# Performance work log

Hardware: AMD Instinct MI355X
Metric: run time of the kernel (lower is better)

Reference implementation:

```python
import jax, jax.numpy as jnp
import numpy as np

N, E, G, H, F_IN = 100_000, 3_200_000, 256, 16, 7
RRELU_SLOPE = (1.0 / 8.0 + 1.0 / 3.0) / 2.0  # eval-mode RReLU uses mean slope


def rrelu(x):
    return jnp.where(x >= 0, x, RRELU_SLOPE * x)


def gcn_conv(x, edge_index, edge_weight, W, b, n_nodes):
    """PyG GCNConv: add self-loops, symmetric norm, gather-matmul-scatter."""
    row, col = edge_index[0], edge_index[1]
    loop = jnp.arange(n_nodes)
    row = jnp.concatenate([row, loop])
    col = jnp.concatenate([col, loop])
    w = jnp.concatenate([edge_weight, jnp.ones((n_nodes,), x.dtype)])
    deg = jax.ops.segment_sum(w, col, num_segments=n_nodes)
    dis = jnp.where(deg > 0, jax.lax.rsqrt(jnp.maximum(deg, 1e-12)), 0.0)
    norm = dis[row] * w * dis[col]            # [E+N]
    h = x @ W                                  # [N, out]
    msg = h[row] * norm[:, None]               # gather + scale
    return jax.ops.segment_sum(msg, col, num_segments=n_nodes) + b


def max_pool_neighbor_x(x, edge_index, n_nodes):
    row, col = edge_index[0], edge_index[1]
    loop = jnp.arange(n_nodes)
    row = jnp.concatenate([row, loop])
    col = jnp.concatenate([col, loop])
    return jax.ops.segment_max(x[row], col, num_segments=n_nodes)


def setup_inputs() -> dict:
    key = jax.random.key(0)
    ks = jax.random.split(key, 12)
    x = jax.random.normal(ks[0], (N, F_IN), jnp.float32)
    edge_index = jax.random.randint(ks[1], (2, E), 0, N)
    edge_weights = jax.random.uniform(ks[2], (E,), jnp.float32)
    batch = (jnp.arange(N) * G) // N  # sorted, every graph non-empty
    s = 0.2
    W1 = jax.random.normal(ks[3], (F_IN, H), jnp.float32) * s
    b1 = jnp.zeros((H,), jnp.float32)
    W2 = jax.random.normal(ks[4], (H, H), jnp.float32) * s
    b2 = jnp.zeros((H,), jnp.float32)
    Wl1 = jax.random.normal(ks[5], (H, H), jnp.float32) * s
    bl1 = jax.random.normal(ks[6], (H,), jnp.float32) * s
    Wl3 = jax.random.normal(ks[7], (H, H), jnp.float32) * s
    bl3 = jax.random.normal(ks[8], (H,), jnp.float32) * s
    Wl4 = jax.random.normal(ks[9], (H, 1), jnp.float32) * s
    bl4 = jax.random.normal(ks[10], (1,), jnp.float32) * s
    return {"x": x, "edge_index": edge_index, "batch": batch,
            "edge_weights": edge_weights, "W1": W1, "b1": b1, "W2": W2,
            "b2": b2, "Wl1": Wl1, "bl1": bl1, "Wl3": Wl3, "bl3": bl3,
            "Wl4": Wl4, "bl4": bl4}


def reference(x, edge_index, batch, edge_weights, W1, b1, W2, b2,
              Wl1, bl1, Wl3, bl3, Wl4, bl4):
    h = gcn_conv(x, edge_index, edge_weights, W1, b1, N)
    h = max_pool_neighbor_x(h, edge_index, N)
    res = h
    h = gcn_conv(h, edge_index, jnp.ones((E,), h.dtype), W2, b2, N)
    h = jax.nn.relu(res + h)
    g = jax.ops.segment_max(h, batch, num_segments=G)  # global_max_pool
    res = g
    g = rrelu(res + (g @ Wl1 + bl1))
    res = g
    g = rrelu(res + (g @ Wl3 + bl3))
    # dropout p=0.5 in eval mode -> identity
    g = rrelu(g @ Wl4 + bl4)
    return g
```

## Files before the change

kernel.cpp:

```cpp
#include <hip/hip_runtime.h>
#include <hip/hip_fp16.h>
#include <math.h>

#define NN 100000
#define NE 3200000
#define NG 256
#define HD 16
#define FIN 7

#define RB 8
#define RSZ 256
#define NBUK 391
#define NBUKP 400
#define FB 1024
#define CHUNK 3125
#define SCB 8
#define ASTRIDE 17
#define CSTRIDE 9
#define LMASK 0x1FFFF

#define S16 65536.0f
#define INV_S16 1.52587890625e-5f
#define IBIAS 33554432u
#define S_DEGW 16777216.0f
#define INV_S_DEGW 5.9604644775390625e-8f

static constexpr float SLOPE = 0.22916666666666666f;

__device__ __forceinline__ float rrelu_f(float a) {
    return a >= 0.f ? a : SLOPE * a;
}

__device__ __forceinline__ unsigned encf(float v) {
    unsigned u = __float_as_uint(v);
    return u ^ (((unsigned)((int)u >> 31)) | 0x80000000u);
}
__device__ __forceinline__ float decf(unsigned u) {
    unsigned m = ((int)u < 0) ? 0x80000000u : 0xFFFFFFFFu;
    return __uint_as_float(u ^ m);
}
#define ENC_NEGINF 0x00800000u

__device__ __forceinline__ float h2f(unsigned short us) {
    __half h = *(__half*)&us;
    return __half2float(h);
}

__global__ __launch_bounds__(256) void k_hist(
        const int* __restrict__ col, int* __restrict__ hist) {
    __shared__ int bins[NBUK];
    for (int i = threadIdx.x; i < NBUK; i += 256) bins[i] = 0;
    __syncthreads();
    int base = blockIdx.x * CHUNK;
    for (int i = threadIdx.x; i < CHUNK; i += 256)
        atomicAdd(&bins[col[base + i] >> RB], 1);
    __syncthreads();
    for (int i = threadIdx.x; i < NBUK; i += 256)
        hist[blockIdx.x * NBUKP + i] = bins[i];
}

__global__ __launch_bounds__(512) void k_scan_a(
        const int* __restrict__ hist, int* __restrict__ pre_t,
        int* __restrict__ tot) {
    __shared__ int s[SCB * (FB + 1)];
    int t = threadIdx.x;
    int c0 = blockIdx.x * SCB;
    for (int i = t; i < SCB * FB; i += 512) {
        int j = i >> 3, c = i & 7;
        int cc = c0 + c;
        s[c * (FB + 1) + j] = (cc < NBUK) ? hist[j * NBUKP + cc] : 0;
    }
    __syncthreads();
    int w = t >> 6, l = t & 63;
    int* sb = &s[w * (FB + 1)];
    int base = l * 16;
    int loc[16];
    int run = 0;
#pragma unroll
    for (int k = 0; k < 16; ++k) { loc[k] = run; run += sb[base + k]; }
    int inc = run;
#pragma unroll
    for (int d = 1; d < 64; d <<= 1) {
        int v = __shfl_up(inc, d, 64);
        if (l >= d) inc += v;
    }
    int excl = inc - run;
    int cc = c0 + w;
    if (cc < NBUK) {
#pragma unroll
        for (int k = 0; k < 16; ++k) sb[base + k] = excl + loc[k];
        if (l == 63) tot[cc] = inc;
    }
    __syncthreads();
    for (int i = t; i < SCB * FB; i += 512) {
        int j = i >> 3, c = i & 7;
        int cc2 = c0 + c;
        if (cc2 < NBUK) pre_t[j * NBUKP + cc2] = s[c * (FB + 1) + j];
    }
}

__global__ __launch_bounds__(512) void k_scan_b(
        const int* __restrict__ tot, int* __restrict__ bstart) {
    __shared__ int s[512];
    int t = threadIdx.x;
    int v = (t < NBUK) ? tot[t] : 0;
    s[t] = v;
    __syncthreads();
    for (int d = 1; d < 512; d <<= 1) {
        int add = (t >= d) ? s[t - d] : 0;
        __syncthreads();
        s[t] += add;
        __syncthreads();
    }
    if (t < NBUK) bstart[t + 1] = s[t];
    if (t == 0) bstart[0] = 0;
}

__global__ __launch_bounds__(256) void k_fill(
        const int* __restrict__ row, const int* __restrict__ col,
        const float* __restrict__ ew,
        const int* __restrict__ pre_t, const int* __restrict__ bstart,
        unsigned* __restrict__ sp, unsigned short* __restrict__ swh) {
    __shared__ int lcnt[NBUK];
    __shared__ int gofs[NBUK];
    __shared__ int part[256];
    __shared__ unsigned ssp[CHUNK];
    __shared__ unsigned short ssw[CHUNK];
    __shared__ unsigned short sbuk[CHUNK];
    int t = threadIdx.x;
    for (int i = t; i < NBUK; i += 256) {
        lcnt[i] = 0;
        gofs[i] = bstart[i] + pre_t[blockIdx.x * NBUKP + i];
    }
    __syncthreads();
    int base = blockIdx.x * CHUNK;
    for (int i = t; i < CHUNK; i += 256)
        atomicAdd(&lcnt[col[base + i] >> RB], 1);
    __syncthreads();
    int k0 = t * 2;
    int c0 = (k0 + 0 < NBUK) ? lcnt[k0 + 0] : 0;
    int c1 = (k0 + 1 < NBUK) ? lcnt[k0 + 1] : 0;
    int gsum = c0 + c1;
    part[t] = gsum;
    __syncthreads();
    for (int d = 1; d < 256; d <<= 1) {
        int add = (t >= d) ? part[t - d] : 0;
        __syncthreads();
        part[t] += add;
        __syncthreads();
    }
    {
        int run = part[t] - gsum;
        int e0 = run, e1 = run + c0;
        if (k0 + 0 < NBUK) { gofs[k0 + 0] -= e0; lcnt[k0 + 0] = e0; }
        if (k0 + 1 < NBUK) { gofs[k0 + 1] -= e1; lcnt[k0 + 1] = e1; }
    }
    __syncthreads();
    for (int i = t; i < CHUNK; i += 256) {
        int c = col[base + i];
        int b = c >> RB;
        int s = atomicAdd(&lcnt[b], 1);
        ssp[s] = ((unsigned)(c & (RSZ - 1)) << 17) | (unsigned)row[base + i];
        __half hv = __float2half_rn(ew[base + i]);
        ssw[s] = *(unsigned short*)&hv;
        sbuk[s] = (unsigned short)b;
    }
    __syncthreads();
    for (int s = t; s < CHUNK; s += 256) {
        int g = s + gofs[sbuk[s]];
        sp[g] = ssp[s];
        swh[g] = ssw[s];
    }
}

__global__ __launch_bounds__(1024) void k_deg(
        const unsigned* __restrict__ sp, const unsigned short* __restrict__ swh,
        const int* __restrict__ bstart,
        const float* __restrict__ x, const float* __restrict__ W1,
        float* __restrict__ h1, float* __restrict__ dis1,
        float* __restrict__ dis2, int* __restrict__ cnts,
        unsigned* __restrict__ h1h) {
    __shared__ unsigned long long sdeg[RSZ];
    __shared__ float sdis[RSZ];
    __shared__ float sW1[FIN * HD];
    int t = threadIdx.x;
    if (t < FIN * HD) sW1[t] = W1[t];
    if (t < RSZ) sdeg[t] = 0ULL;
    __syncthreads();
    int s0 = bstart[blockIdx.x], s1 = bstart[blockIdx.x + 1];
    int j = s0 + t;
    for (; j + 3072 < s1; j += 4096) {
        unsigned e0 = sp[j], e1 = sp[j + 1024], e2 = sp[j + 2048], e3 = sp[j + 3072];
        float w0 = h2f(swh[j]), w1 = h2f(swh[j + 1024]);
        float w2 = h2f(swh[j + 2048]), w3 = h2f(swh[j + 3072]);
        atomicAdd(&sdeg[e0 >> 17], (1ULL << 32) |
                  (unsigned long long)(unsigned)__float2int_rn(w0 * S_DEGW));
        atomicAdd(&sdeg[e1 >> 17], (1ULL << 32) |
                  (unsigned long long)(unsigned)__float2int_rn(w1 * S_DEGW));
        atomicAdd(&sdeg[e2 >> 17], (1ULL << 32) |
                  (unsigned long long)(unsigned)__float2int_rn(w2 * S_DEGW));
        atomicAdd(&sdeg[e3 >> 17], (1ULL << 32) |
                  (unsigned long long)(unsigned)__float2int_rn(w3 * S_DEGW));
    }
    for (; j < s1; j += 1024) {
        unsigned e = sp[j];
        float w = h2f(swh[j]);
        atomicAdd(&sdeg[e >> 17], (1ULL << 32) |
                  (unsigned long long)(unsigned)__float2int_rn(w * S_DEGW));
    }
    __syncthreads();
    int node0 = blockIdx.x * RSZ;
    if (t < RSZ && node0 + t < NN) {
        unsigned long long v = sdeg[t];
        unsigned cnt = (unsigned)(v >> 32);
        float wsum = (float)(unsigned)(v & 0xFFFFFFFFULL) * INV_S_DEGW;
        float d1 = rsqrtf(wsum + 1.f);
        dis1[node0 + t] = d1;
        sdis[t] = d1;
        dis2[node0 + t] = rsqrtf((float)cnt + 1.f);
        cnts[node0 + t] = (int)cnt;
    }
    __syncthreads();
    for (int i = t; i < RSZ * 8; i += 1024) {
        int ln = i >> 3, p = i & 7;
        int node = node0 + ln;
        if (node < NN) {
            float a0 = 0.f, a1 = 0.f;
#pragma unroll
            for (int k = 0; k < FIN; ++k) {
                float xv = x[node * FIN + k];
                a0 += xv * sW1[k * HD + 2 * p];
                a1 += xv * sW1[k * HD + 2 * p + 1];
            }
            h1[node * HD + 2 * p] = a0;
            h1[node * HD + 2 * p + 1] = a1;
            float d = sdis[ln];
            __half2 hh = __floats2half2_rn(a0 * d, a1 * d);
            h1h[node * 8 + p] = *(unsigned*)&hh;
        }
    }
}

__device__ __forceinline__ void conv_acc2(unsigned long long* acc, unsigned ex,
                                          uint2 g, float w, int p2) {
    float2 fa = __half22float2(*(__half2*)&g.x);
    float2 fb = __half22float2(*(__half2*)&g.y);
    unsigned qa0 = (unsigned)__float2int_rn(fa.x * w) + IBIAS;
    unsigned qa1 = (unsigned)__float2int_rn(fa.y * w) + IBIAS;
    unsigned qb0 = (unsigned)__float2int_rn(fb.x * w) + IBIAS;
    unsigned qb1 = (unsigned)__float2int_rn(fb.y * w) + IBIAS;
    int lc = ex >> 17;
    atomicAdd(&acc[lc * CSTRIDE + 2 * p2],
              ((unsigned long long)qa0 << 32) | (unsigned long long)qa1);
    atomicAdd(&acc[lc * CSTRIDE + 2 * p2 + 1],
              ((unsigned long long)qb0 << 32) | (unsigned long long)qb1);
}

__global__ __launch_bounds__(1024) void k_conv1(
        const unsigned* __restrict__ sp, const unsigned short* __restrict__ swh,
        const int* __restrict__ bstart,
        const unsigned* __restrict__ h1h, const float* __restrict__ h1,
        const float* __restrict__ dis1, const int* __restrict__ cnts,
        const float* __restrict__ b1, unsigned* __restrict__ h1outh) {
    __shared__ unsigned long long acc[RSZ * CSTRIDE];
    int t = threadIdx.x;
    for (int i = t; i < RSZ * CSTRIDE; i += 1024) acc[i] = 0ULL;
    __syncthreads();
    int p2 = t & 3, slot = t >> 2;
    const uint2* h1h2 = (const uint2*)h1h;
    int s0 = bstart[blockIdx.x], s1 = bstart[blockIdx.x + 1];
    int j = s0 + slot;
    for (; j + 768 < s1; j += 1024) {
        unsigned e0 = sp[j], e1 = sp[j + 256], e2 = sp[j + 512], e3 = sp[j + 768];
        float w0 = h2f(swh[j]) * S16, w1 = h2f(swh[j + 256]) * S16;
        float w2 = h2f(swh[j + 512]) * S16, w3 = h2f(swh[j + 768]) * S16;
        uint2 g0 = h1h2[(e0 & LMASK) * 4 + p2];
        uint2 g1 = h1h2[(e1 & LMASK) * 4 + p2];
        uint2 g2 = h1h2[(e2 & LMASK) * 4 + p2];
        uint2 g3 = h1h2[(e3 & LMASK) * 4 + p2];
        conv_acc2(acc, e0, g0, w0, p2);
        conv_acc2(acc, e1, g1, w1, p2);
        conv_acc2(acc, e2, g2, w2, p2);
        conv_acc2(acc, e3, g3, w3, p2);
    }
    for (; j < s1; j += 256) {
        unsigned e = sp[j];
        float w = h2f(swh[j]) * S16;
        uint2 g = h1h2[(e & LMASK) * 4 + p2];
        conv_acc2(acc, e, g, w, p2);
    }
    __syncthreads();
    int node0 = blockIdx.x * RSZ;
    for (int i = t; i < RSZ * 8; i += 1024) {
        int ln = i >> 3, pp = i & 7;
        int node = node0 + ln;
        if (node < NN) {
            unsigned long long v = acc[ln * CSTRIDE + pp];
            unsigned kb = (unsigned)cnts[node] * IBIAS;
            float a0 = (float)(int)((unsigned)(v >> 32) - kb) * INV_S16;
            float a1 = (float)(int)((unsigned)(v & 0xFFFFFFFFULL) - kb) * INV_S16;
            float d = dis1[node];
            float r0 = a0 * d + h1[node * HD + 2 * pp] * d * d + b1[2 * pp];
            float r1 = a1 * d + h1[node * HD + 2 * pp + 1] * d * d + b1[2 * pp + 1];
            __half2 hh = __floats2half2_rn(r0, r1);
            h1outh[node * 8 + pp] = *(unsigned*)&hh;
        }
    }
}

__global__ __launch_bounds__(1024) void k_pool_h2(
        const unsigned* __restrict__ sp, const int* __restrict__ bstart,
        const unsigned* __restrict__ h1outh, const float* __restrict__ W2,
        const float* __restrict__ dis2,
        float2* __restrict__ pool2, float2* __restrict__ h2s,
        unsigned* __restrict__ h2sh) {
    __shared__ unsigned acc[RSZ * ASTRIDE];
    __shared__ float sW2[256];
    int t = threadIdx.x;
    if (t < 256) sW2[t] = W2[t];
    for (int i = t; i < RSZ * ASTRIDE; i += 1024) acc[i] = ENC_NEGINF;
    __syncthreads();
    int p2 = t & 3, slot = t >> 2;
    const uint2* hv2 = (const uint2*)h1outh;
    int s0 = bstart[blockIdx.x], s1 = bstart[blockIdx.x + 1];
    int j = s0 + slot;
    for (; j + 768 < s1; j += 1024) {
        unsigned e0 = sp[j], e1 = sp[j + 256], e2 = sp[j + 512], e3 = sp[j + 768];
        uint2 g0 = hv2[(e0 & LMASK) * 4 + p2];
        uint2 g1 = hv2[(e1 & LMASK) * 4 + p2];
        uint2 g2 = hv2[(e2 & LMASK) * 4 + p2];
        uint2 g3 = hv2[(e3 & LMASK) * 4 + p2];
        float2 f;
        unsigned* a;
        a = &acc[(e0 >> 17) * ASTRIDE + 4 * p2];
        f = __half22float2(*(__half2*)&g0.x);
        atomicMax(a + 0, encf(f.x)); atomicMax(a + 1, encf(f.y));
        f = __half22float2(*(__half2*)&g0.y);
        atomicMax(a + 2, encf(f.x)); atomicMax(a + 3, encf(f.y));
        a = &acc[(e1 >> 17) * ASTRIDE + 4 * p2];
        f = __half22float2(*(__half2*)&g1.x);
        atomicMax(a + 0, encf(f.x)); atomicMax(a + 1, encf(f.y));
        f = __half22float2(*(__half2*)&g1.y);
        atomicMax(a + 2, encf(f.x)); atomicMax(a + 3, encf(f.y));
        a = &acc[(e2 >> 17) * ASTRIDE + 4 * p2];
        f = __half22float2(*(__half2*)&g2.x);
        atomicMax(a + 0, encf(f.x)); atomicMax(a + 1, encf(f.y));
        f = __half22float2(*(__half2*)&g2.y);
        atomicMax(a + 2, encf(f.x)); atomicMax(a + 3, encf(f.y));
        a = &acc[(e3 >> 17) * ASTRIDE + 4 * p2];
        f = __half22float2(*(__half2*)&g3.x);
        atomicMax(a + 0, encf(f.x)); atomicMax(a + 1, encf(f.y));
        f = __half22float2(*(__half2*)&g3.y);
        atomicMax(a + 2, encf(f.x)); atomicMax(a + 3, encf(f.y));
    }
    for (; j < s1; j += 256) {
        unsigned e = sp[j];
        uint2 g = hv2[(e & LMASK) * 4 + p2];
        unsigned* a = &acc[(e >> 17) * ASTRIDE + 4 * p2];
        float2 f = __half22float2(*(__half2*)&g.x);
        atomicMax(a + 0, encf(f.x)); atomicMax(a + 1, encf(f.y));
        f = __half22float2(*(__half2*)&g.y);
        atomicMax(a + 2, encf(f.x)); atomicMax(a + 3, encf(f.y));
    }
    __syncthreads();
    int node0 = blockIdx.x * RSZ;
    for (int i = t; i < RSZ * 8; i += 1024) {
        int ln = i >> 3, pp = i & 7;
        int node = node0 + ln;
        if (node < NN) {
            unsigned sh = h1outh[node * 8 + pp];
            float2 sf = __half22float2(*(__half2*)&sh);
            float m0 = fmaxf(decf(acc[ln * ASTRIDE + 2 * pp]),     sf.x);
            float m1 = fmaxf(decf(acc[ln * ASTRIDE + 2 * pp + 1]), sf.y);
            pool2[node * 8 + pp] = make_float2(m0, m1);
            acc[ln * ASTRIDE + 2 * pp]     = __float_as_uint(m0);
            acc[ln * ASTRIDE + 2 * pp + 1] = __float_as_uint(m1);
        }
    }
    __syncthreads();
    for (int i = t; i < RSZ * 8; i += 1024) {
        int ln = i >> 3, pp = i & 7;
        int node = node0 + ln;
        if (node < NN) {
            float a0 = 0.f, a1 = 0.f;
#pragma unroll
            for (int k = 0; k < HD; ++k) {
                float pv = __uint_as_float(acc[ln * ASTRIDE + k]);
                a0 += pv * sW2[k * HD + 2 * pp];
                a1 += pv * sW2[k * HD + 2 * pp + 1];
            }
            float d = dis2[node];
            a0 *= d; a1 *= d;
            h2s[node * 8 + pp] = make_float2(a0, a1);
            __half2 hh = __floats2half2_rn(a0, a1);
            h2sh[node * 8 + pp] = *(unsigned*)&hh;
        }
    }
}

__global__ __launch_bounds__(1024) void k_conv2(
        const unsigned* __restrict__ sp, const int* __restrict__ bstart,
        const unsigned* __restrict__ h2sh, const float2* __restrict__ h2s,
        const float* __restrict__ dis2, const int* __restrict__ cnts,
        const float2* __restrict__ pool2, const float* __restrict__ b2,
        float2* __restrict__ hfin2) {
    __shared__ unsigned long long acc[RSZ * CSTRIDE];
    int t = threadIdx.x;
    for (int i = t; i < RSZ * CSTRIDE; i += 1024) acc[i] = 0ULL;
    __syncthreads();
    int p2 = t & 3, slot = t >> 2;
    const uint2* hv2 = (const uint2*)h2sh;
    int s0 = bstart[blockIdx.x], s1 = bstart[blockIdx.x + 1];
    int j = s0 + slot;
    for (; j + 768 < s1; j += 1024) {
        unsigned e0 = sp[j], e1 = sp[j + 256], e2 = sp[j + 512], e3 = sp[j + 768];
        uint2 g0 = hv2[(e0 & LMASK) * 4 + p2];
        uint2 g1 = hv2[(e1 & LMASK) * 4 + p2];
        uint2 g2 = hv2[(e2 & LMASK) * 4 + p2];
        uint2 g3 = hv2[(e3 & LMASK) * 4 + p2];
        conv_acc2(acc, e0, g0, S16, p2);
        conv_acc2(acc, e1, g1, S16, p2);
        conv_acc2(acc, e2, g2, S16, p2);
        conv_acc2(acc, e3, g3, S16, p2);
    }
    for (; j < s1; j += 256) {
        unsigned e = sp[j];
        uint2 g = hv2[(e & LMASK) * 4 + p2];
        conv_acc2(acc, e, g, S16, p2);
    }
    __syncthreads();
    int node0 = blockIdx.x * RSZ;
    for (int i = t; i < RSZ * 8; i += 1024) {
        int ln = i >> 3, pp = i & 7;
        int node = node0 + ln;
        if (node < NN) {
            unsigned long long v = acc[ln * CSTRIDE + pp];
            unsigned kb = (unsigned)cnts[node] * IBIAS;
            float a0 = (float)(int)((unsigned)(v >> 32) - kb) * INV_S16;
            float a1 = (float)(int)((unsigned)(v & 0xFFFFFFFFULL) - kb) * INV_S16;
            float d = dis2[node];
            float2 self = h2s[node * 8 + pp];
            float2 pl = pool2[node * 8 + pp];
            float r0 = pl.x + (a0 + self.x) * d + b2[2 * pp];
            float r1 = pl.y + (a1 + self.y) * d + b2[2 * pp + 1];
            hfin2[node * 8 + pp] = make_float2(fmaxf(r0, 0.f), fmaxf(r1, 0.f));
        }
    }
}

__global__ __launch_bounds__(256) void k_graph_max(
        const float* __restrict__ hfin, float* __restrict__ gbuf) {
    int g = blockIdx.x;
    int start = (g * NN + NG - 1) / NG;
    int end   = ((g + 1) * NN + NG - 1) / NG;
    int f = threadIdx.x & 15, sub = threadIdx.x >> 4;
    float m = -3.402823466e38f;
    for (int i = start + sub; i < end; i += 16)
        m = fmaxf(m, hfin[i * HD + f]);
    __shared__ float lds[256];
    lds[threadIdx.x] = m;
    __syncthreads();
    if (threadIdx.x < 16) {
        float mm = lds[threadIdx.x];
#pragma unroll
        for (int s = 1; s < 16; ++s) mm = fmaxf(mm, lds[s * 16 + threadIdx.x]);
        gbuf[g * HD + threadIdx.x] = mm;
    }
}

__global__ __launch_bounds__(256) void k_mlp(
        const float* __restrict__ gbuf,
        const float* __restrict__ Wl1, const float* __restrict__ bl1,
        const float* __restrict__ Wl3, const float* __restrict__ bl3,
        const float* __restrict__ Wl4, const float* __restrict__ bl4,
        float* __restrict__ out) {
    __shared__ float sW1[256], sW3[256], sW4[16], sb1[16], sb3[16];
    __shared__ float sb4;
    int tid = threadIdx.x;
    sW1[tid] = Wl1[tid];
    sW3[tid] = Wl3[tid];
    if (tid < 16) { sW4[tid] = Wl4[tid]; sb1[tid] = bl1[tid]; sb3[tid] = bl3[tid]; }
    if (tid == 0) sb4 = bl4[0];
    __syncthreads();

    float v[16], t1[16], t2[16];
#pragma unroll
    for (int f = 0; f < 16; ++f) v[f] = gbuf[tid * 16 + f];
#pragma unroll
    for (int f = 0; f < 16; ++f) {
        float a = sb1[f] + v[f];
#pragma unroll
        for (int k = 0; k < 16; ++k) a += v[k] * sW1[k * 16 + f];
        t1[f] = rrelu_f(a);
    }
#pragma unroll
    for (int f = 0; f < 16; ++f) {
        float a = sb3[f] + t1[f];
#pragma unroll
        for (int k = 0; k < 16; ++k) a += t1[k] * sW3[k * 16 + f];
        t2[f] = rrelu_f(a);
    }
    float o = sb4;
#pragma unroll
    for (int k = 0; k < 16; ++k) o += t2[k] * sW4[k];
    out[tid] = rrelu_f(o);
}

extern "C" void kernel_launch(void* const* d_in, const int* in_sizes, int n_in,
                              void* d_out, int out_size, void* d_ws, size_t ws_size,
                              hipStream_t stream) {
    const float* x   = (const float*)d_in[0];
    const int*   ei  = (const int*)  d_in[1];
    const float* ew  = (const float*)d_in[3];
    const float* W1  = (const float*)d_in[4];
    const float* b1  = (const float*)d_in[5];
    const float* W2  = (const float*)d_in[6];
    const float* b2  = (const float*)d_in[7];
    const float* Wl1 = (const float*)d_in[8];
    const float* bl1 = (const float*)d_in[9];
    const float* Wl3 = (const float*)d_in[10];
    const float* bl3 = (const float*)d_in[11];
    const float* Wl4 = (const float*)d_in[12];
    const float* bl4 = (const float*)d_in[13];
    const int* row = ei;
    const int* col = ei + NE;

    float* ws = (float*)d_ws;
    float* h1    = ws;
    float* pool  = h1   + NN * HD;
    float* h2s   = pool + NN * HD;
    float* dis1  = h2s  + NN * HD;
    float* dis2  = dis1 + NN;
    int*   cnts  = (int*)(dis2 + NN);
    float* gbuf  = (float*)(cnts + NN);
    unsigned* h1h    = (unsigned*)(gbuf + NG * HD);
    unsigned* h1outh = h1h    + NN * 8;
    unsigned* h2sh   = h1outh + NN * 8;
    unsigned* sp     = h2sh   + NN * 8;
    unsigned short* swh = (unsigned short*)(sp + NE);
    int* tot    = (int*)(swh + NE + (NE & 1));
    int* bstart = tot + NBUK;
    int* hist   = (int*)pool;
    int* pre_t  = (int*)h2s;
    float* hfin = h1;

    const int B = 256;

    k_hist     <<<FB, B, 0, stream>>>(col, hist);
    k_scan_a   <<<(NBUK + SCB - 1) / SCB, 512, 0, stream>>>(hist, pre_t, tot);
    k_scan_b   <<<1, 512, 0, stream>>>(tot, bstart);
    k_fill     <<<FB, B, 0, stream>>>(row, col, ew, pre_t, bstart, sp, swh);
    k_deg      <<<NBUK, 1024, 0, stream>>>(sp, swh, bstart, x, W1, h1,
                                           dis1, dis2, cnts, h1h);
    k_conv1    <<<NBUK, 1024, 0, stream>>>(sp, swh, bstart, h1h, h1, dis1,
                                           cnts, b1, h1outh);
    k_pool_h2  <<<NBUK, 1024, 0, stream>>>(sp, bstart, h1outh, W2, dis2,
                                           (float2*)pool, (float2*)h2s, h2sh);
    k_conv2    <<<NBUK, 1024, 0, stream>>>(sp, bstart, h2sh, (const float2*)h2s, dis2,
                                           cnts, (const float2*)pool, b2, (float2*)hfin);
    k_graph_max<<<NG, B, 0, stream>>>(hfin, gbuf);
    k_mlp      <<<1, B, 0, stream>>>(gbuf, Wl1, bl1, Wl3, bl3, Wl4, bl4, (float*)d_out);
}
```

Baseline: 259.5 us.

## Build per-node CSR and replace LDS atomic aggregation with per-node register reductions

After: 316.8 us. 22.1% more time.

```diff
diff --git a/kernel.cpp b/kernel.cpp
--- a/kernel.cpp
+++ b/kernel.cpp
@@ -16,12 +16,8 @@
 #define CHUNK 3125
 #define SCB 8
 #define ASTRIDE 17
-#define CSTRIDE 9
 #define LMASK 0x1FFFF
 
-#define S16 65536.0f
-#define INV_S16 1.52587890625e-5f
-#define IBIAS 33554432u
 #define S_DEGW 16777216.0f
 #define INV_S_DEGW 5.9604644775390625e-8f
 
@@ -30,16 +26,6 @@
 __device__ __forceinline__ float rrelu_f(float a) {
     return a >= 0.f ? a : SLOPE * a;
 }
-
-__device__ __forceinline__ unsigned encf(float v) {
-    unsigned u = __float_as_uint(v);
-    return u ^ (((unsigned)((int)u >> 31)) | 0x80000000u);
-}
-__device__ __forceinline__ float decf(unsigned u) {
-    unsigned m = ((int)u < 0) ? 0x80000000u : 0xFFFFFFFFu;
-    return __uint_as_float(u ^ m);
-}
-#define ENC_NEGINF 0x00800000u
 
 __device__ __forceinline__ float h2f(unsigned short us) {
     __half h = *(__half*)&us;
@@ -173,279 +159,233 @@
     }
 }
 
-__global__ __launch_bounds__(1024) void k_deg(
+__global__ __launch_bounds__(1024) void k_sort2(
         const unsigned* __restrict__ sp, const unsigned short* __restrict__ swh,
         const int* __restrict__ bstart,
         const float* __restrict__ x, const float* __restrict__ W1,
-        float* __restrict__ h1, float* __restrict__ dis1,
-        float* __restrict__ dis2, int* __restrict__ cnts,
-        unsigned* __restrict__ h1h) {
-    __shared__ unsigned long long sdeg[RSZ];
+        unsigned* __restrict__ sp2, unsigned short* __restrict__ sw2,
+        int* __restrict__ rowptr, float* __restrict__ dis1,
+        float* __restrict__ dis2, unsigned* __restrict__ h1h) {
+    __shared__ int scnt[RSZ];
+    __shared__ int stmp[RSZ];
+    __shared__ int soff[RSZ + 1];
+    __shared__ int walker[RSZ];
+    __shared__ unsigned wsum[RSZ];
     __shared__ float sdis[RSZ];
     __shared__ float sW1[FIN * HD];
     int t = threadIdx.x;
     if (t < FIN * HD) sW1[t] = W1[t];
-    if (t < RSZ) sdeg[t] = 0ULL;
+    if (t < RSZ) { scnt[t] = 0; walker[t] = 0; wsum[t] = 0u; }
     __syncthreads();
     int s0 = bstart[blockIdx.x], s1 = bstart[blockIdx.x + 1];
-    int j = s0 + t;
-    for (; j + 3072 < s1; j += 4096) {
-        unsigned e0 = sp[j], e1 = sp[j + 1024], e2 = sp[j + 2048], e3 = sp[j + 3072];
-        float w0 = h2f(swh[j]), w1 = h2f(swh[j + 1024]);
-        float w2 = h2f(swh[j + 2048]), w3 = h2f(swh[j + 3072]);
-        atomicAdd(&sdeg[e0 >> 17], (1ULL << 32) |
-                  (unsigned long long)(unsigned)__float2int_rn(w0 * S_DEGW));
-        atomicAdd(&sdeg[e1 >> 17], (1ULL << 32) |
-                  (unsigned long long)(unsigned)__float2int_rn(w1 * S_DEGW));
-        atomicAdd(&sdeg[e2 >> 17], (1ULL << 32) |
-                  (unsigned long long)(unsigned)__float2int_rn(w2 * S_DEGW));
-        atomicAdd(&sdeg[e3 >> 17], (1ULL << 32) |
-                  (unsigned long long)(unsigned)__float2int_rn(w3 * S_DEGW));
-    }
-    for (; j < s1; j += 1024) {
+    for (int j = s0 + t; j < s1; j += 1024)
+        atomicAdd(&scnt[sp[j] >> 17], 1);
+    __syncthreads();
+    int c = (t < RSZ) ? scnt[t] : 0;
+    if (t < RSZ) stmp[t] = c;
+    __syncthreads();
+    for (int d = 1; d < RSZ; d <<= 1) {
+        int v = (t < RSZ && t >= d) ? stmp[t - d] : 0;
+        __syncthreads();
+        if (t < RSZ) stmp[t] += v;
+        __syncthreads();
+    }
+    if (t < RSZ) soff[t] = stmp[t] - c;
+    if (t == 0) soff[RSZ] = s1 - s0;
+    __syncthreads();
+    int node0 = blockIdx.x * RSZ;
+    for (int i = t; i <= RSZ; i += 1024) {
+        int node = node0 + i;
+        if (node <= NN) rowptr[node] = s0 + soff[i];
+    }
+    for (int j = s0 + t; j < s1; j += 1024) {
         unsigned e = sp[j];
-        float w = h2f(swh[j]);
-        atomicAdd(&sdeg[e >> 17], (1ULL << 32) |
-                  (unsigned long long)(unsigned)__float2int_rn(w * S_DEGW));
-    }
-    __syncthreads();
-    int node0 = blockIdx.x * RSZ;
-    if (t < RSZ && node0 + t < NN) {
-        unsigned long long v = sdeg[t];
-        unsigned cnt = (unsigned)(v >> 32);
-        float wsum = (float)(unsigned)(v & 0xFFFFFFFFULL) * INV_S_DEGW;
-        float d1 = rsqrtf(wsum + 1.f);
-        dis1[node0 + t] = d1;
-        sdis[t] = d1;
-        dis2[node0 + t] = rsqrtf((float)cnt + 1.f);
-        cnts[node0 + t] = (int)cnt;
-    }
-    __syncthreads();
-    for (int i = t; i < RSZ * 8; i += 1024) {
-        int ln = i >> 3, p = i & 7;
+        unsigned short w = swh[j];
+        int lc = e >> 17;
+        int pos = s0 + soff[lc] + atomicAdd(&walker[lc], 1);
+        sp2[pos] = e & LMASK;
+        sw2[pos] = w;
+        atomicAdd(&wsum[lc], (unsigned)__float2int_rn(h2f(w) * S_DEGW));
+    }
+    __syncthreads();
+    if (t < RSZ) {
+        int node = node0 + t;
+        if (node < NN) {
+            float wsumf = (float)wsum[t] * INV_S_DEGW;
+            float d1 = rsqrtf(wsumf + 1.f);
+            dis1[node] = d1;
+            sdis[t] = d1;
+            dis2[node] = rsqrtf((float)scnt[t] + 1.f);
+        }
+    }
+    __syncthreads();
+    uint2* h1h2 = (uint2*)h1h;
+    for (int i = t; i < RSZ * 4; i += 1024) {
+        int ln = i >> 2, p2 = i & 3;
         int node = node0 + ln;
         if (node < NN) {
-            float a0 = 0.f, a1 = 0.f;
+            float a0 = 0.f, a1 = 0.f, a2 = 0.f, a3 = 0.f;
 #pragma unroll
             for (int k = 0; k < FIN; ++k) {
                 float xv = x[node * FIN + k];
-                a0 += xv * sW1[k * HD + 2 * p];
-                a1 += xv * sW1[k * HD + 2 * p + 1];
+                a0 += xv * sW1[k * HD + 4 * p2 + 0];
+                a1 += xv * sW1[k * HD + 4 * p2 + 1];
+                a2 += xv * sW1[k * HD + 4 * p2 + 2];
+                a3 += xv * sW1[k * HD + 4 * p2 + 3];
             }
-            h1[node * HD + 2 * p] = a0;
-            h1[node * HD + 2 * p + 1] = a1;
             float d = sdis[ln];
-            __half2 hh = __floats2half2_rn(a0 * d, a1 * d);
-            h1h[node * 8 + p] = *(unsigned*)&hh;
+            __half2 ha = __floats2half2_rn(a0 * d, a1 * d);
+            __half2 hb = __floats2half2_rn(a2 * d, a3 * d);
+            h1h2[node * 4 + p2] = make_uint2(*(unsigned*)&ha, *(unsigned*)&hb);
         }
     }
 }
 
-__device__ __forceinline__ void conv_acc2(unsigned long long* acc, unsigned ex,
-                                          uint2 g, float w, int p2) {
-    float2 fa = __half22float2(*(__half2*)&g.x);
-    float2 fb = __half22float2(*(__half2*)&g.y);
-    unsigned qa0 = (unsigned)__float2int_rn(fa.x * w) + IBIAS;
-    unsigned qa1 = (unsigned)__float2int_rn(fa.y * w) + IBIAS;
-    unsigned qb0 = (unsigned)__float2int_rn(fb.x * w) + IBIAS;
-    unsigned qb1 = (unsigned)__float2int_rn(fb.y * w) + IBIAS;
-    int lc = ex >> 17;
-    atomicAdd(&acc[lc * CSTRIDE + 2 * p2],
-              ((unsigned long long)qa0 << 32) | (unsigned long long)qa1);
-    atomicAdd(&acc[lc * CSTRIDE + 2 * p2 + 1],
-              ((unsigned long long)qb0 << 32) | (unsigned long long)qb1);
-}
+#define ACCW(g, w) { \
+    float2 fa_ = __half22float2(*(__half2*)&(g).x); \
+    float2 fb_ = __half22float2(*(__half2*)&(g).y); \
+    a0 += fa_.x * (w); a1 += fa_.y * (w); a2 += fb_.x * (w); a3 += fb_.y * (w); }
+
+#define ACCS(g) { \
+    float2 fa_ = __half22float2(*(__half2*)&(g).x); \
+    float2 fb_ = __half22float2(*(__half2*)&(g).y); \
+    a0 += fa_.x; a1 += fa_.y; a2 += fb_.x; a3 += fb_.y; }
+
+#define ACCM(g) { \
+    float2 fa_ = __half22float2(*(__half2*)&(g).x); \
+    float2 fb_ = __half22float2(*(__half2*)&(g).y); \
+    a0 = fmaxf(a0, fa_.x); a1 = fmaxf(a1, fa_.y); \
+    a2 = fmaxf(a2, fb_.x); a3 = fmaxf(a3, fb_.y); }
 
 __global__ __launch_bounds__(1024) void k_conv1(
-        const unsigned* __restrict__ sp, const unsigned short* __restrict__ swh,
-        const int* __restrict__ bstart,
-        const unsigned* __restrict__ h1h, const float* __restrict__ h1,
-        const float* __restrict__ dis1, const int* __restrict__ cnts,
+        const unsigned* __restrict__ sp2, const unsigned short* __restrict__ sw2,
+        const int* __restrict__ rowptr,
+        const unsigned* __restrict__ h1h, const float* __restrict__ dis1,
         const float* __restrict__ b1, unsigned* __restrict__ h1outh) {
-    __shared__ unsigned long long acc[RSZ * CSTRIDE];
-    int t = threadIdx.x;
-    for (int i = t; i < RSZ * CSTRIDE; i += 1024) acc[i] = 0ULL;
-    __syncthreads();
-    int p2 = t & 3, slot = t >> 2;
-    const uint2* h1h2 = (const uint2*)h1h;
-    int s0 = bstart[blockIdx.x], s1 = bstart[blockIdx.x + 1];
-    int j = s0 + slot;
-    for (; j + 768 < s1; j += 1024) {
-        unsigned e0 = sp[j], e1 = sp[j + 256], e2 = sp[j + 512], e3 = sp[j + 768];
-        float w0 = h2f(swh[j]) * S16, w1 = h2f(swh[j + 256]) * S16;
-        float w2 = h2f(swh[j + 512]) * S16, w3 = h2f(swh[j + 768]) * S16;
-        uint2 g0 = h1h2[(e0 & LMASK) * 4 + p2];
-        uint2 g1 = h1h2[(e1 & LMASK) * 4 + p2];
-        uint2 g2 = h1h2[(e2 & LMASK) * 4 + p2];
-        uint2 g3 = h1h2[(e3 & LMASK) * 4 + p2];
-        conv_acc2(acc, e0, g0, w0, p2);
-        conv_acc2(acc, e1, g1, w1, p2);
-        conv_acc2(acc, e2, g2, w2, p2);
-        conv_acc2(acc, e3, g3, w3, p2);
-    }
-    for (; j < s1; j += 256) {
-        unsigned e = sp[j];
-        float w = h2f(swh[j]) * S16;
-        uint2 g = h1h2[(e & LMASK) * 4 + p2];
-        conv_acc2(acc, e, g, w, p2);
+    int t = threadIdx.x;
+    int ln = t >> 2, p2 = t & 3;
+    int node = blockIdx.x * RSZ + ln;
+    if (node >= NN) return;
+    const uint2* hv = (const uint2*)h1h;
+    int r0 = rowptr[node], r1 = rowptr[node + 1];
+    float a0 = 0.f, a1 = 0.f, a2 = 0.f, a3 = 0.f;
+    int r = r0;
+    for (; r + 3 < r1; r += 4) {
+        unsigned n0 = sp2[r], n1 = sp2[r + 1], n2 = sp2[r + 2], n3 = sp2[r + 3];
+        float w0 = h2f(sw2[r]),     w1 = h2f(sw2[r + 1]);
+        float w2 = h2f(sw2[r + 2]), w3 = h2f(sw2[r + 3]);
+        uint2 g0 = hv[n0 * 4 + p2], g1 = hv[n1 * 4 + p2];
+        uint2 g2 = hv[n2 * 4 + p2], g3 = hv[n3 * 4 + p2];
+        ACCW(g0, w0); ACCW(g1, w1); ACCW(g2, w2); ACCW(g3, w3);
+    }
+    for (; r < r1; ++r) {
+        unsigned n = sp2[r];
+        float w = h2f(sw2[r]);
+        uint2 g = hv[n * 4 + p2];
+        ACCW(g, w);
+    }
+    uint2 gs = hv[node * 4 + p2];
+    float2 sa = __half22float2(*(__half2*)&gs.x);
+    float2 sb = __half22float2(*(__half2*)&gs.y);
+    float d = dis1[node];
+    float o0 = (a0 + sa.x) * d + b1[4 * p2 + 0];
+    float o1 = (a1 + sa.y) * d + b1[4 * p2 + 1];
+    float o2 = (a2 + sb.x) * d + b1[4 * p2 + 2];
+    float o3 = (a3 + sb.y) * d + b1[4 * p2 + 3];
+    __half2 ha = __floats2half2_rn(o0, o1);
+    __half2 hb = __floats2half2_rn(o2, o3);
+    ((uint2*)h1outh)[node * 4 + p2] = make_uint2(*(unsigned*)&ha, *(unsigned*)&hb);
+}
+
+__global__ __launch_bounds__(1024) void k_pool_h2(
+        const unsigned* __restrict__ sp2, const int* __restrict__ rowptr,
+        const unsigned* __restrict__ h1outh, const float* __restrict__ W2,
+        const float* __restrict__ dis2,
+        float4* __restrict__ pool4, unsigned* __restrict__ h2sh) {
+    __shared__ float spool[RSZ * ASTRIDE];
+    __shared__ float sW2[256];
+    int t = threadIdx.x;
+    if (t < 256) sW2[t] = W2[t];
+    int ln = t >> 2, p2 = t & 3;
+    int node = blockIdx.x * RSZ + ln;
+    const uint2* hv = (const uint2*)h1outh;
+    if (node < NN) {
+        uint2 gs = hv[node * 4 + p2];
+        float2 sa = __half22float2(*(__half2*)&gs.x);
+        float2 sb = __half22float2(*(__half2*)&gs.y);
+        float a0 = sa.x, a1 = sa.y, a2 = sb.x, a3 = sb.y;
+        int r0 = rowptr[node], r1 = rowptr[node + 1];
+        int r = r0;
+        for (; r + 3 < r1; r += 4) {
+            unsigned n0 = sp2[r], n1 = sp2[r + 1], n2 = sp2[r + 2], n3 = sp2[r + 3];
+            uint2 g0 = hv[n0 * 4 + p2], g1 = hv[n1 * 4 + p2];
+            uint2 g2 = hv[n2 * 4 + p2], g3 = hv[n3 * 4 + p2];
+            ACCM(g0); ACCM(g1); ACCM(g2); ACCM(g3);
+        }
+        for (; r < r1; ++r) {
+            uint2 g = hv[sp2[r] * 4 + p2];
+            ACCM(g);
+        }
+        pool4[node * 4 + p2] = make_float4(a0, a1, a2, a3);
+        spool[ln * ASTRIDE + 4 * p2 + 0] = a0;
+        spool[ln * ASTRIDE + 4 * p2 + 1] = a1;
+        spool[ln * ASTRIDE + 4 * p2 + 2] = a2;
+        spool[ln * ASTRIDE + 4 * p2 + 3] = a3;
     }
     __syncthreads();
     int node0 = blockIdx.x * RSZ;
     for (int i = t; i < RSZ * 8; i += 1024) {
-        int ln = i >> 3, pp = i & 7;
-        int node = node0 + ln;
-        if (node < NN) {
-            unsigned long long v = acc[ln * CSTRIDE + pp];
-            unsigned kb = (unsigned)cnts[node] * IBIAS;
-            float a0 = (float)(int)((unsigned)(v >> 32) - kb) * INV_S16;
-            float a1 = (float)(int)((unsigned)(v & 0xFFFFFFFFULL) - kb) * INV_S16;
-            float d = dis1[node];
-            float r0 = a0 * d + h1[node * HD + 2 * pp] * d * d + b1[2 * pp];
-            float r1 = a1 * d + h1[node * HD + 2 * pp + 1] * d * d + b1[2 * pp + 1];
-            __half2 hh = __floats2half2_rn(r0, r1);
-            h1outh[node * 8 + pp] = *(unsigned*)&hh;
-        }
-    }
-}
-
-__global__ __launch_bounds__(1024) void k_pool_h2(
-        const unsigned* __restrict__ sp, const int* __restrict__ bstart,
-        const unsigned* __restrict__ h1outh, const float* __restrict__ W2,
-        const float* __restrict__ dis2,
-        float2* __restrict__ pool2, float2* __restrict__ h2s,
-        unsigned* __restrict__ h2sh) {
-    __shared__ unsigned acc[RSZ * ASTRIDE];
-    __shared__ float sW2[256];
-    int t = threadIdx.x;
-    if (t < 256) sW2[t] = W2[t];
-    for (int i = t; i < RSZ * ASTRIDE; i += 1024) acc[i] = ENC_NEGINF;
-    __syncthreads();
-    int p2 = t & 3, slot = t >> 2;
-    const uint2* hv2 = (const uint2*)h1outh;
-    int s0 = bstart[blockIdx.x], s1 = bstart[blockIdx.x + 1];
-    int j = s0 + slot;
-    for (; j + 768 < s1; j += 1024) {
-        unsigned e0 = sp[j], e1 = sp[j + 256], e2 = sp[j + 512], e3 = sp[j + 768];
-        uint2 g0 = hv2[(e0 & LMASK) * 4 + p2];
-        uint2 g1 = hv2[(e1 & LMASK) * 4 + p2];
-        uint2 g2 = hv2[(e2 & LMASK) * 4 + p2];
-        uint2 g3 = hv2[(e3 & LMASK) * 4 + p2];
-        float2 f;
-        unsigned* a;
-        a = &acc[(e0 >> 17) * ASTRIDE + 4 * p2];
-        f = __half22float2(*(__half2*)&g0.x);
-        atomicMax(a + 0, encf(f.x)); atomicMax(a + 1, encf(f.y));
-        f = __half22float2(*(__half2*)&g0.y);
-        atomicMax(a + 2, encf(f.x)); atomicMax(a + 3, encf(f.y));
-        a = &acc[(e1 >> 17) * ASTRIDE + 4 * p2];
-        f = __half22float2(*(__half2*)&g1.x);
-        atomicMax(a + 0, encf(f.x)); atomicMax(a + 1, encf(f.y));
-        f = __half22float2(*(__half2*)&g1.y);
-        atomicMax(a + 2, encf(f.x)); atomicMax(a + 3, encf(f.y));
-        a = &acc[(e2 >> 17) * ASTRIDE + 4 * p2];
-        f = __half22float2(*(__half2*)&g2.x);
-        atomicMax(a + 0, encf(f.x)); atomicMax(a + 1, encf(f.y));
-        f = __half22float2(*(__half2*)&g2.y);
-        atomicMax(a + 2, encf(f.x)); atomicMax(a + 3, encf(f.y));
-        a = &acc[(e3 >> 17) * ASTRIDE + 4 * p2];
-        f = __half22float2(*(__half2*)&g3.x);
-        atomicMax(a + 0, encf(f.x)); atomicMax(a + 1, encf(f.y));
-        f = __half22float2(*(__half2*)&g3.y);
-        atomicMax(a + 2, encf(f.x)); atomicMax(a + 3, encf(f.y));
-    }
-    for (; j < s1; j += 256) {
-        unsigned e = sp[j];
-        uint2 g = hv2[(e & LMASK) * 4 + p2];
-        unsigned* a = &acc[(e >> 17) * ASTRIDE + 4 * p2];
-        float2 f = __half22float2(*(__half2*)&g.x);
-        atomicMax(a + 0, encf(f.x)); atomicMax(a + 1, encf(f.y));
-        f = __half22float2(*(__half2*)&g.y);
-        atomicMax(a + 2, encf(f.x)); atomicMax(a + 3, encf(f.y));
-    }
-    __syncthreads();
-    int node0 = blockIdx.x * RSZ;
-    for (int i = t; i < RSZ * 8; i += 1024) {
-        int ln = i >> 3, pp = i & 7;
-        int node = node0 + ln;
-        if (node < NN) {
-            unsigned sh = h1outh[node * 8 + pp];
-            float2 sf = __half22float2(*(__half2*)&sh);
-            float m0 = fmaxf(decf(acc[ln * ASTRIDE + 2 * pp]),     sf.x);
-            float m1 = fmaxf(decf(acc[ln * ASTRIDE + 2 * pp + 1]), sf.y);
-            pool2[node * 8 + pp] = make_float2(m0, m1);
-            acc[ln * ASTRIDE + 2 * pp]     = __float_as_uint(m0);
-            acc[ln * ASTRIDE + 2 * pp + 1] = __float_as_uint(m1);
-        }
-    }
-    __syncthreads();
-    for (int i = t; i < RSZ * 8; i += 1024) {
-        int ln = i >> 3, pp = i & 7;
-        int node = node0 + ln;
-        if (node < NN) {
+        int l2 = i >> 3, pp = i & 7;
+        int nd = node0 + l2;
+        if (nd < NN) {
             float a0 = 0.f, a1 = 0.f;
 #pragma unroll
             for (int k = 0; k < HD; ++k) {
-                float pv = __uint_as_float(acc[ln * ASTRIDE + k]);
+                float pv = spool[l2 * ASTRIDE + k];
                 a0 += pv * sW2[k * HD + 2 * pp];
                 a1 += pv * sW2[k * HD + 2 * pp + 1];
             }
-            float d = dis2[node];
-            a0 *= d; a1 *= d;
-            h2s[node * 8 + pp] = make_float2(a0, a1);
-            __half2 hh = __floats2half2_rn(a0, a1);
-            h2sh[node * 8 + pp] = *(unsigned*)&hh;
+            float dd = dis2[nd];
+            __half2 hh = __floats2half2_rn(a0 * dd, a1 * dd);
+            h2sh[nd * 8 + pp] = *(unsigned*)&hh;
         }
     }
 }
 
 __global__ __launch_bounds__(1024) void k_conv2(
-        const unsigned* __restrict__ sp, const int* __restrict__ bstart,
-        const unsigned* __restrict__ h2sh, const float2* __restrict__ h2s,
-        const float* __restrict__ dis2, const int* __restrict__ cnts,
-        const float2* __restrict__ pool2, const float* __restrict__ b2,
-        float2* __restrict__ hfin2) {
-    __shared__ unsigned long long acc[RSZ * CSTRIDE];
-    int t = threadIdx.x;
-    for (int i = t; i < RSZ * CSTRIDE; i += 1024) acc[i] = 0ULL;
-    __syncthreads();
-    int p2 = t & 3, slot = t >> 2;
-    const uint2* hv2 = (const uint2*)h2sh;
-    int s0 = bstart[blockIdx.x], s1 = bstart[blockIdx.x + 1];
-    int j = s0 + slot;
-    for (; j + 768 < s1; j += 1024) {
-        unsigned e0 = sp[j], e1 = sp[j + 256], e2 = sp[j + 512], e3 = sp[j + 768];
-        uint2 g0 = hv2[(e0 & LMASK) * 4 + p2];
-        uint2 g1 = hv2[(e1 & LMASK) * 4 + p2];
-        uint2 g2 = hv2[(e2 & LMASK) * 4 + p2];
-        uint2 g3 = hv2[(e3 & LMASK) * 4 + p2];
-        conv_acc2(acc, e0, g0, S16, p2);
-        conv_acc2(acc, e1, g1, S16, p2);
-        conv_acc2(acc, e2, g2, S16, p2);
-        conv_acc2(acc, e3, g3, S16, p2);
-    }
-    for (; j < s1; j += 256) {
-        unsigned e = sp[j];
-        uint2 g = hv2[(e & LMASK) * 4 + p2];
-        conv_acc2(acc, e, g, S16, p2);
-    }
-    __syncthreads();
-    int node0 = blockIdx.x * RSZ;
-    for (int i = t; i < RSZ * 8; i += 1024) {
-        int ln = i >> 3, pp = i & 7;
-        int node = node0 + ln;
-        if (node < NN) {
-            unsigned long long v = acc[ln * CSTRIDE + pp];
-            unsigned kb = (unsigned)cnts[node] * IBIAS;
-            float a0 = (float)(int)((unsigned)(v >> 32) - kb) * INV_S16;
-            float a1 = (float)(int)((unsigned)(v & 0xFFFFFFFFULL) - kb) * INV_S16;
-            float d = dis2[node];
-            float2 self = h2s[node * 8 + pp];
-            float2 pl = pool2[node * 8 + pp];
-            float r0 = pl.x + (a0 + self.x) * d + b2[2 * pp];
-            float r1 = pl.y + (a1 + self.y) * d + b2[2 * pp + 1];
-            hfin2[node * 8 + pp] = make_float2(fmaxf(r0, 0.f), fmaxf(r1, 0.f));
-        }
-    }
+        const unsigned* __restrict__ sp2, const int* __restrict__ rowptr,
+        const unsigned* __restrict__ h2sh, const float* __restrict__ dis2,
+        const float4* __restrict__ pool4, const float* __restrict__ b2,
+        float4* __restrict__ hfin4) {
+    int t = threadIdx.x;
+    int ln = t >> 2, p2 = t & 3;
+    int node = blockIdx.x * RSZ + ln;
+    if (node >= NN) return;
+    const uint2* hv = (const uint2*)h2sh;
+    int r0 = rowptr[node], r1 = rowptr[node + 1];
+    float a0 = 0.f, a1 = 0.f, a2 = 0.f, a3 = 0.f;
+    int r = r0;
+    for (; r + 3 < r1; r += 4) {
+        unsigned n0 = sp2[r], n1 = sp2[r + 1], n2 = sp2[r + 2], n3 = sp2[r + 3];
+        uint2 g0 = hv[n0 * 4 + p2], g1 = hv[n1 * 4 + p2];
+        uint2 g2 = hv[n2 * 4 + p2], g3 = hv[n3 * 4 + p2];
+        ACCS(g0); ACCS(g1); ACCS(g2); ACCS(g3);
+    }
+    for (; r < r1; ++r) {
+        uint2 g = hv[sp2[r] * 4 + p2];
+        ACCS(g);
+    }
+    uint2 gs = hv[node * 4 + p2];
+    float2 sa = __half22float2(*(__half2*)&gs.x);
+    float2 sb = __half22float2(*(__half2*)&gs.y);
+    float d = dis2[node];
+    float4 pl = pool4[node * 4 + p2];
+    float o0 = pl.x + (a0 + sa.x) * d + b2[4 * p2 + 0];
+    float o1 = pl.y + (a1 + sa.y) * d + b2[4 * p2 + 1];
+    float o2 = pl.z + (a2 + sb.x) * d + b2[4 * p2 + 2];
+    float o3 = pl.w + (a3 + sb.y) * d + b2[4 * p2 + 3];
+    hfin4[node * 4 + p2] = make_float4(fmaxf(o0, 0.f), fmaxf(o1, 0.f),
+                                       fmaxf(o2, 0.f), fmaxf(o3, 0.f));
 }
 
 __global__ __launch_bounds__(256) void k_graph_max(
@@ -525,24 +465,24 @@
     const int* row = ei;
     const int* col = ei + NE;
 
-    float* ws = (float*)d_ws;
-    float* h1    = ws;
-    float* pool  = h1   + NN * HD;
-    float* h2s   = pool + NN * HD;
-    float* dis1  = h2s  + NN * HD;
-    float* dis2  = dis1 + NN;
-    int*   cnts  = (int*)(dis2 + NN);
-    float* gbuf  = (float*)(cnts + NN);
-    unsigned* h1h    = (unsigned*)(gbuf + NG * HD);
-    unsigned* h1outh = h1h    + NN * 8;
-    unsigned* h2sh   = h1outh + NN * 8;
-    unsigned* sp     = h2sh   + NN * 8;
+    unsigned* sp2 = (unsigned*)d_ws;
+    unsigned short* sw2 = (unsigned short*)(sp2 + NE);
+    unsigned* h1h = (unsigned*)(sw2 + NE);
+    int* rowptr = (int*)(h1h + NN * 8);
+    float* dis1 = (float*)(rowptr + NN + 4);
+    float* dis2 = dis1 + NN;
+    float* gbuf = dis2 + NN;
+    unsigned* regA = (unsigned*)(gbuf + NG * HD);
+    int* hist  = (int*)sp2;
+    int* pre_t = hist + FB * NBUKP;
+    unsigned* sp = regA;
     unsigned short* swh = (unsigned short*)(sp + NE);
-    int* tot    = (int*)(swh + NE + (NE & 1));
+    unsigned* h1outh = regA;
+    float* pool = (float*)(regA + NN * 8);
+    unsigned* h2sh = (unsigned*)(pool + NN * 16);
+    float* hfin = (float*)(h2sh + NN * 8);
+    int* tot = (int*)(regA + NE + NE / 2);
     int* bstart = tot + NBUK;
-    int* hist   = (int*)pool;
-    int* pre_t  = (int*)h2s;
-    float* hfin = h1;
 
     const int B = 256;
 
@@ -550,14 +490,13 @@
     k_scan_a   <<<(NBUK + SCB - 1) / SCB, 512, 0, stream>>>(hist, pre_t, tot);
     k_scan_b   <<<1, 512, 0, stream>>>(tot, bstart);
     k_fill     <<<FB, B, 0, stream>>>(row, col, ew, pre_t, bstart, sp, swh);
-    k_deg      <<<NBUK, 1024, 0, stream>>>(sp, swh, bstart, x, W1, h1,
-                                           dis1, dis2, cnts, h1h);
-    k_conv1    <<<NBUK, 1024, 0, stream>>>(sp, swh, bstart, h1h, h1, dis1,
-                                           cnts, b1, h1outh);
-    k_pool_h2  <<<NBUK, 1024, 0, stream>>>(sp, bstart, h1outh, W2, dis2,
-                                           (float2*)pool, (float2*)h2s, h2sh);
-    k_conv2    <<<NBUK, 1024, 0, stream>>>(sp, bstart, h2sh, (const float2*)h2s, dis2,
-                                           cnts, (const float2*)pool, b2, (float2*)hfin);
+    k_sort2    <<<NBUK, 1024, 0, stream>>>(sp, swh, bstart, x, W1,
+                                           sp2, sw2, rowptr, dis1, dis2, h1h);
+    k_conv1    <<<NBUK, 1024, 0, stream>>>(sp2, sw2, rowptr, h1h, dis1, b1, h1outh);
+    k_pool_h2  <<<NBUK, 1024, 0, stream>>>(sp2, rowptr, h1outh, W2, dis2,
+                                           (float4*)pool, h2sh);
+    k_conv2    <<<NBUK, 1024, 0, stream>>>(sp2, rowptr, h2sh, dis2,
+                                           (const float4*)pool, b2, (float4*)hfin);
     k_graph_max<<<NG, B, 0, stream>>>(hfin, gbuf);
     k_mlp      <<<1, B, 0, stream>>>(gbuf, Wl1, bl1, Wl3, bl3, Wl4, bl4, (float*)d_out);
 }
```
